# Kernel tuning notes

Hardware: AMD Instinct MI355X
Metric: run time of the kernel (lower is better)

The kernel has to match this reference:

```python
import jax, jax.numpy as jnp
import numpy as np

B, L, D, N = 4, 4096, 1024, 1024  # d_state must equal d_model for the original broadcasting to work


def _bayes_linear(x, wmu, wlv, bmu, blv, key):
    """Reparameterized Bayesian linear: w = mu + exp(0.5*log_var)*eps."""
    kw, kb = jax.random.split(key)
    w = wmu + jnp.exp(0.5 * wlv) * jax.random.normal(kw, wmu.shape, wmu.dtype)
    b = bmu + jnp.exp(0.5 * blv) * jax.random.normal(kb, bmu.shape, bmu.dtype)
    return x @ w.T + b


def setup_inputs() -> dict:
    key = jax.random.key(0)
    ks = jax.random.split(key, 17)
    inp = {"x": jax.random.normal(ks[0], (B, L, D), jnp.float32)}
    shapes = {"A": (N, D), "Bp": (N, D), "C": (D, N), "dt": (N, D)}
    i = 1
    for name, (o, ii) in shapes.items():
        # torch init: mu ~ N(0, 0.1), log_var ~ N(-9, 0.1)
        inp[f"{name}_wmu"] = 0.1 * jax.random.normal(ks[i], (o, ii), jnp.float32); i += 1
        inp[f"{name}_wlv"] = -9.0 + 0.1 * jax.random.normal(ks[i], (o, ii), jnp.float32); i += 1
        inp[f"{name}_bmu"] = 0.1 * jax.random.normal(ks[i], (o,), jnp.float32); i += 1
        inp[f"{name}_blv"] = -9.0 + 0.1 * jax.random.normal(ks[i], (o,), jnp.float32); i += 1
    return inp


def reference(x, A_wmu, A_wlv, A_bmu, A_blv,
              Bp_wmu, Bp_wlv, Bp_bmu, Bp_blv,
              C_wmu, C_wlv, C_bmu, C_blv,
              dt_wmu, dt_wlv, dt_bmu, dt_blv):
    key = jax.random.key(42)
    kA, kB, kC, kdt = jax.random.split(key, 4)
    A = -jnp.exp(_bayes_linear(x, A_wmu, A_wlv, A_bmu, A_blv, kA))   # [B,L,N]
    dt = jnp.exp(_bayes_linear(x, dt_wmu, dt_wlv, dt_bmu, dt_blv, kdt))
    Bm = _bayes_linear(x, Bp_wmu, Bp_wlv, Bp_bmu, Bp_blv, kB)        # [B,L,N]
    C = _bayes_linear(x, C_wmu, C_wlv, C_bmu, C_blv, kC)             # [B,L,D]

    E = jnp.exp(A * dt)   # per-step decay, [B,L,N]
    Bx = Bm * x           # input injection (requires N == D, as in original)

    def step(h, inp):
        e, bx, c = inp
        h = h * e + bx
        return h, c * h

    ET = jnp.swapaxes(E, 0, 1)    # time-major [L,B,N]
    BxT = jnp.swapaxes(Bx, 0, 1)
    CT = jnp.swapaxes(C, 0, 1)
    h0 = jnp.zeros((x.shape[0], N), x.dtype)
    _, yT = jax.lax.scan(step, h0, (ET, BxT, CT))
    # The torch code broadcasts h to [B,B,N] and sums over dim=1; h is identical
    # along that axis, so the sum equals multiplying by batch_size.
    return jnp.swapaxes(yT, 0, 1) * x.shape[0]
```

## Files before the change

kernel.cpp:

```cpp
#include <hip/hip_runtime.h>
#include <cstdint>

__host__ __device__ inline void tf2x32(uint32_t k0, uint32_t k1,
                                       uint32_t x0, uint32_t x1,
                                       uint32_t& o0, uint32_t& o1) {
  uint32_t ks2 = k0 ^ k1 ^ 0x1BD11BDAu;
  uint32_t v0 = x0 + k0, v1 = x1 + k1;
#define TFR(r) { v0 += v1; v1 = (v1 << r) | (v1 >> (32 - r)); v1 ^= v0; }
  TFR(13) TFR(15) TFR(26) TFR(6)
  v0 += k1;  v1 += ks2 + 1u;
  TFR(17) TFR(29) TFR(16) TFR(24)
  v0 += ks2; v1 += k0 + 2u;
  TFR(13) TFR(15) TFR(26) TFR(6)
  v0 += k0;  v1 += k1 + 3u;
  TFR(17) TFR(29) TFR(16) TFR(24)
  v0 += k1;  v1 += ks2 + 4u;
  TFR(13) TFR(15) TFR(26) TFR(6)
  v0 += ks2; v1 += k0 + 5u;
#undef TFR
  o0 = v0; o1 = v1;
}

__device__ inline float erfinv32(float x) {
  float w = -log1pf(-x * x);
  float p;
  if (w < 5.0f) {
    w -= 2.5f;
    p = 2.81022636e-08f;
    p = fmaf(p, w, 3.43273939e-07f);
    p = fmaf(p, w, -3.5233877e-06f);
    p = fmaf(p, w, -4.39150654e-06f);
    p = fmaf(p, w, 0.00021858087f);
    p = fmaf(p, w, -0.00125372503f);
    p = fmaf(p, w, -0.00417768164f);
    p = fmaf(p, w, 0.246640727f);
    p = fmaf(p, w, 1.50140941f);
  } else {
    w = sqrtf(w) - 3.0f;
    p = -0.000200214257f;
    p = fmaf(p, w, 0.000100950558f);
    p = fmaf(p, w, 0.00134934322f);
    p = fmaf(p, w, -0.00367342844f);
    p = fmaf(p, w, 0.00573950773f);
    p = fmaf(p, w, -0.0076224613f);
    p = fmaf(p, w, 0.00943887047f);
    p = fmaf(p, w, 1.00167406f);
    p = fmaf(p, w, 2.83297682f);
  }
  return p * x;
}

__device__ inline float rng_normal(uint32_t k0, uint32_t k1, uint32_t idx) {
  uint32_t o0, o1;
  tf2x32(k0, k1, 0u, idx, o0, o1);
  uint32_t bits = o0 ^ o1;
  float f = __uint_as_float((bits >> 9) | 0x3f800000u) - 1.0f;
  const float lo = -0.999999940395355224609375f;
  float u = fmaxf(lo, f * 2.0f + lo);
  return 1.41421356237f * erfinv32(u);
}

struct RngKeys {
  uint32_t wA0, wA1, bA0, bA1;
  uint32_t wB0, wB1, bB0, bB1;
  uint32_t wC0, wC1, bC0, bC1;
  uint32_t wD0, wD1, bD0, bD1;
};

typedef _Float16 f16x8 __attribute__((ext_vector_type(8)));
typedef _Float16 f16x4 __attribute__((ext_vector_type(4)));
typedef float f32x4 __attribute__((ext_vector_type(4)));

__global__ __launch_bounds__(256) void gen_weights(
    const float* __restrict__ Awmu, const float* __restrict__ Awlv,
    const float* __restrict__ Dwmu, const float* __restrict__ Dwlv,
    const float* __restrict__ Bwmu, const float* __restrict__ Bwlv,
    const float* __restrict__ Cwmu, const float* __restrict__ Cwlv,
    _Float16* __restrict__ Wh, RngKeys kk) {
  uint32_t idx = blockIdx.x * 256u + threadIdx.x;
  uint32_t sel = idx >> 20;
  uint32_t e = idx & 0xFFFFFu;
  float w;
  if (sel == 0u) {
    w = Awmu[e] + expf(0.5f * Awlv[e]) * rng_normal(kk.wA0, kk.wA1, e)
      + Dwmu[e] + expf(0.5f * Dwlv[e]) * rng_normal(kk.wD0, kk.wD1, e);
  } else if (sel == 1u) {
    w = Bwmu[e] + expf(0.5f * Bwlv[e]) * rng_normal(kk.wB0, kk.wB1, e);
  } else {
    w = Cwmu[e] + expf(0.5f * Cwlv[e]) * rng_normal(kk.wC0, kk.wC1, e);
  }
  Wh[idx] = (_Float16)w;
}

__global__ __launch_bounds__(256) void gen_bias(
    const float* __restrict__ Abmu, const float* __restrict__ Ablv,
    const float* __restrict__ Dbmu, const float* __restrict__ Dblv,
    const float* __restrict__ Bbmu, const float* __restrict__ Bblv,
    const float* __restrict__ Cbmu, const float* __restrict__ Cblv,
    float* __restrict__ bcat, RngKeys kk) {
  uint32_t o = blockIdx.x * 256u + threadIdx.x;
  uint32_t e = o & 1023u;
  float b;
  if (o < 1024u)
    b = Abmu[e] + expf(0.5f * Ablv[e]) * rng_normal(kk.bA0, kk.bA1, e)
      + Dbmu[e] + expf(0.5f * Dblv[e]) * rng_normal(kk.bD0, kk.bD1, e);
  else if (o < 2048u)
    b = Bbmu[e] + expf(0.5f * Bblv[e]) * rng_normal(kk.bB0, kk.bB1, e);
  else
    b = Cbmu[e] + expf(0.5f * Cblv[e]) * rng_normal(kk.bC0, kk.bC1, e);
  bcat[o] = b;
}

__global__ __launch_bounds__(256) void convert_x(const float* __restrict__ X,
                                                 _Float16* __restrict__ Xh) {
  size_t i4 = ((size_t)blockIdx.x * 256 + threadIdx.x) * 4;
  float4 v = *(const float4*)(X + i4);
  f16x4 h;
  h[0] = (_Float16)v.x; h[1] = (_Float16)v.y;
  h[2] = (_Float16)v.z; h[3] = (_Float16)v.w;
  *(f16x4*)(Xh + i4) = h;
}

__device__ inline void gl2lds16(const void* g, void* l) {
  __builtin_amdgcn_global_load_lds(
      (const __attribute__((address_space(1))) void*)g,
      (__attribute__((address_space(3))) void*)l, 16, 0, 0);
}

__global__ __launch_bounds__(256, 4) void gemm_fused(
    const _Float16* __restrict__ Xh, const _Float16* __restrict__ Wh,
    const float* __restrict__ X, const float* __restrict__ bcat,
    _Float16* __restrict__ Z, float* __restrict__ out) {
  __shared__ _Float16 sA[128 * 32];
  __shared__ _Float16 sB[128 * 32];

  const int tid = threadIdx.x;
  const int m0 = blockIdx.y * 128;
  const int n0 = blockIdx.x * 128;

  const int srow = tid >> 2;
  const int scg = (tid & 3) ^ ((srow >> 1) & 3);
  const _Float16* gA = Xh + (size_t)(m0 + srow) * 1024 + scg * 8;
  const _Float16* gB = Wh + (size_t)(n0 + srow) * 1024 + scg * 8;
  char* lA = (char*)sA + tid * 16;
  char* lB = (char*)sB + tid * 16;

  const int lane = tid & 63;
  const int wave = tid >> 6;
  const int wm = wave >> 1, wn = wave & 1;
  const int fr = lane & 15;
  const int q = lane >> 4;
  const int kc = q ^ ((fr >> 1) & 3);

  f32x4 acc[4][4] = {};

  for (int k0 = 0; k0 < 1024; k0 += 32) {
    __syncthreads();
    gl2lds16(gA + k0, lA);
    gl2lds16(gA + 64 * 1024 + k0, lA + 4096);
    gl2lds16(gB + k0, lB);
    gl2lds16(gB + 64 * 1024 + k0, lB + 4096);
    __syncthreads();

    f16x8 ah[4], bh[4];
#pragma unroll
    for (int t = 0; t < 4; ++t) {
      int ar = (wm * 64 + t * 16 + fr) * 32 + kc * 8;
      int br = (wn * 64 + t * 16 + fr) * 32 + kc * 8;
      ah[t] = *(const f16x8*)&sA[ar];
      bh[t] = *(const f16x8*)&sB[br];
    }
#pragma unroll
    for (int mt = 0; mt < 4; ++mt)
#pragma unroll
      for (int nt = 0; nt < 4; ++nt)
        acc[mt][nt] = __builtin_amdgcn_mfma_f32_16x16x32_f16(
            ah[mt], bh[nt], acc[mt][nt], 0, 0, 0);
  }

  const int seg = n0 >> 10;
  const int mrow = (lane >> 4) * 4;
#pragma unroll
  for (int nt = 0; nt < 4; ++nt) {
    int n = n0 + wn * 64 + nt * 16 + fr;
    float bv = bcat[n];
#pragma unroll
    for (int mt = 0; mt < 4; ++mt) {
      int mbase = m0 + wm * 64 + mt * 16 + mrow;
      f32x4 a = acc[mt][nt];
#pragma unroll
      for (int r = 0; r < 4; ++r) {
        int m = mbase + r;
        float v = a[r] + bv;
        if (seg == 0) {
          Z[(size_t)m * 2048 + n] = (_Float16)expf(-expf(v));
        } else if (seg == 1) {
          Z[(size_t)m * 2048 + n] =
              (_Float16)(v * X[(size_t)m * 1024 + (n - 1024)]);
        } else {
          out[(size_t)m * 1024 + (n - 2048)] = v;
        }
      }
    }
  }
}

#define LSEQ 4096
#define NC 64
#define LC 64
#define ZW 2048

__global__ __launch_bounds__(256) void scan_chunk(const _Float16* __restrict__ Z,
                                                  float* __restrict__ ac,
                                                  float* __restrict__ uc) {
  int n = blockIdx.x * 256 + threadIdx.x;
  int c = blockIdx.y;
  int b = blockIdx.z;
  const _Float16* base = Z + (size_t)(b * LSEQ + c * LC) * ZW;
  float a = 1.0f, u = 0.0f;
#pragma unroll 4
  for (int l = 0; l < LC; ++l) {
    float e  = (float)base[(size_t)l * ZW + n];
    float bx = (float)base[(size_t)l * ZW + 1024 + n];
    a *= e;
    u = fmaf(e, u, bx);
  }
  size_t o = ((size_t)b * NC + c) * 1024 + n;
  ac[o] = a;
  uc[o] = u;
}

__global__ __launch_bounds__(256) void scan_prefix(const float* __restrict__ ac,
                                                   const float* __restrict__ uc,
                                                   float* __restrict__ hin) {
  int idx = blockIdx.x * 256 + threadIdx.x;
  int b = idx >> 10, n = idx & 1023;
  float h = 0.0f;
  for (int c = 0; c < NC; ++c) {
    size_t o = ((size_t)b * NC + c) * 1024 + n;
    hin[o] = h;
    h = fmaf(ac[o], h, uc[o]);
  }
}

__global__ __launch_bounds__(256) void scan_final(const _Float16* __restrict__ Z,
                                                  const float* __restrict__ hin,
                                                  float* __restrict__ out) {
  int n = blockIdx.x * 256 + threadIdx.x;
  int c = blockIdx.y;
  int b = blockIdx.z;
  const _Float16* base = Z + (size_t)(b * LSEQ + c * LC) * ZW;
  float* obase = out + (size_t)(b * LSEQ + c * LC) * 1024;
  float h = hin[((size_t)b * NC + c) * 1024 + n];
#pragma unroll 4
  for (int l = 0; l < LC; ++l) {
    float e  = (float)base[(size_t)l * ZW + n];
    float bx = (float)base[(size_t)l * ZW + 1024 + n];
    float cc = obase[(size_t)l * 1024 + n];
    h = fmaf(e, h, bx);
    obase[(size_t)l * 1024 + n] = cc * h * 4.0f;
  }
}

extern "C" void kernel_launch(void* const* d_in, const int* in_sizes, int n_in,
                              void* d_out, int out_size, void* d_ws, size_t ws_size,
                              hipStream_t stream) {
  const float* x    = (const float*)d_in[0];
  const float* Awmu = (const float*)d_in[1];
  const float* Awlv = (const float*)d_in[2];
  const float* Abmu = (const float*)d_in[3];
  const float* Ablv = (const float*)d_in[4];
  const float* Bwmu = (const float*)d_in[5];
  const float* Bwlv = (const float*)d_in[6];
  const float* Bbmu = (const float*)d_in[7];
  const float* Bblv = (const float*)d_in[8];
  const float* Cwmu = (const float*)d_in[9];
  const float* Cwlv = (const float*)d_in[10];
  const float* Cbmu = (const float*)d_in[11];
  const float* Cblv = (const float*)d_in[12];
  const float* Dwmu = (const float*)d_in[13];
  const float* Dwlv = (const float*)d_in[14];
  const float* Dbmu = (const float*)d_in[15];
  const float* Dblv = (const float*)d_in[16];

  uint32_t k4[4][2];
  for (uint32_t i = 0; i < 4; ++i)
    tf2x32(0u, 42u, 0u, i, k4[i][0], k4[i][1]);
  RngKeys kk;
  tf2x32(k4[0][0], k4[0][1], 0u, 0u, kk.wA0, kk.wA1);
  tf2x32(k4[0][0], k4[0][1], 0u, 1u, kk.bA0, kk.bA1);
  tf2x32(k4[1][0], k4[1][1], 0u, 0u, kk.wB0, kk.wB1);
  tf2x32(k4[1][0], k4[1][1], 0u, 1u, kk.bB0, kk.bB1);
  tf2x32(k4[2][0], k4[2][1], 0u, 0u, kk.wC0, kk.wC1);
  tf2x32(k4[2][0], k4[2][1], 0u, 1u, kk.bC0, kk.bC1);
  tf2x32(k4[3][0], k4[3][1], 0u, 0u, kk.wD0, kk.wD1);
  tf2x32(k4[3][0], k4[3][1], 0u, 1u, kk.bD0, kk.bD1);

  char* ws = (char*)d_ws;
  const size_t OFF_WH   = 0;
  const size_t OFF_BCAT = 6291456;
  const size_t OFF_XH   = 8388608;
  const size_t OFF_Z    = 41943040;
  const size_t OFF_AC   = OFF_Z + (size_t)16384 * 2048 * 2;
  const size_t OFF_UC   = OFF_AC + (size_t)4 * NC * 1024 * 4;
  const size_t OFF_HIN  = OFF_UC + (size_t)4 * NC * 1024 * 4;
  const size_t NEEDED   = OFF_HIN + (size_t)4 * NC * 1024 * 4;
  if (ws_size < NEEDED) return;

  _Float16* Wh  = (_Float16*)(ws + OFF_WH);
  float*    bcat= (float*)(ws + OFF_BCAT);
  _Float16* Xh  = (_Float16*)(ws + OFF_XH);
  _Float16* Z   = (_Float16*)(ws + OFF_Z);
  float*    ac  = (float*)(ws + OFF_AC);
  float*    ucv = (float*)(ws + OFF_UC);
  float*    hin = (float*)(ws + OFF_HIN);
  float*    out = (float*)d_out;

  gen_weights<<<dim3(12288), dim3(256), 0, stream>>>(
      Awmu, Awlv, Dwmu, Dwlv, Bwmu, Bwlv, Cwmu, Cwlv, Wh, kk);
  gen_bias<<<dim3(12), dim3(256), 0, stream>>>(
      Abmu, Ablv, Dbmu, Dblv, Bbmu, Bblv, Cbmu, Cblv, bcat, kk);
  convert_x<<<dim3(16384), dim3(256), 0, stream>>>(x, Xh);
  gemm_fused<<<dim3(24, 128), dim3(256), 0, stream>>>(
      Xh, Wh, x, bcat, Z, out);
  scan_chunk<<<dim3(4, NC, 4), dim3(256), 0, stream>>>(Z, ac, ucv);
  scan_prefix<<<dim3(16), dim3(256), 0, stream>>>(ac, ucv, hin);
  scan_final<<<dim3(4, NC, 4), dim3(256), 0, stream>>>(Z, hin, out);
}
```

Measured before the change: 390.0 us.

## Restructure fused GEMM into 256x256 double-buffered tiles with ping-pong MFMA schedule

The projection GEMM moves from 128x128 tiles with BK=32 and one LDS buffer to 256x256 tiles with BK=64, double-buffered LDS and 512 threads per block. Each k-step is split into four MFMA quadrants, with global-to-LDS prefetch of the next tile interleaved, explicit barriers and setprio to overlap memory and matrix work. A block-index swizzle improves L2 reuse across tiles. The aim is higher arithmetic intensity and hidden load latency. The cost is 128KB of LDS per block, which caps occupancy at one block per CU, plus higher register pressure from the larger accumulator.

```diff
diff --git a/kernel.cpp b/kernel.cpp
--- a/kernel.cpp
+++ b/kernel.cpp
@@ -127,71 +127,152 @@
       (__attribute__((address_space(3))) void*)l, 16, 0, 0);
 }
 
-__global__ __launch_bounds__(256, 4) void gemm_fused(
+#define STAGE_T(S, GP, BUF, KT1)                              \
+  do {                                                        \
+    const _Float16* g_ = (GP) + (KT1) * 64;                   \
+    char* l_ = (char*)(&S[(BUF)][0]) + tid * 16;              \
+    gl2lds16(g_,              l_);                            \
+    gl2lds16(g_ +  64 * 1024, l_ + 8192);                     \
+    gl2lds16(g_ + 128 * 1024, l_ + 16384);                    \
+    gl2lds16(g_ + 192 * 1024, l_ + 24576);                    \
+  } while (0)
+
+#define READ_A(MH)                                                      \
+  do {                                                                  \
+    _Pragma("unroll") for (int k_ = 0; k_ < 4; ++k_) {                  \
+      const int ro_ = abase + ((MH) * 4 + k_) * 1024;                   \
+      ah[2 * k_]     = *(const f16x8*)&sA[cur][ro_ + apos];             \
+      ah[2 * k_ + 1] = *(const f16x8*)&sA[cur][ro_ + (apos ^ 32)];      \
+    }                                                                   \
+  } while (0)
+
+#define READ_B(NH)                                                      \
+  do {                                                                  \
+    _Pragma("unroll") for (int j_ = 0; j_ < 2; ++j_) {                  \
+      const int ro_ = bbase + ((NH) * 2 + j_) * 1024;                   \
+      bh[2 * j_]     = *(const f16x8*)&sB[cur][ro_ + apos];             \
+      bh[2 * j_ + 1] = *(const f16x8*)&sB[cur][ro_ + (apos ^ 32)];      \
+    }                                                                   \
+  } while (0)
+
+#define DO_MFMA(MH, NH)                                                      \
+  do {                                                                       \
+    _Pragma("unroll") for (int k_ = 0; k_ < 4; ++k_) {                       \
+      _Pragma("unroll") for (int j_ = 0; j_ < 2; ++j_) {                     \
+        f32x4 c_ = acc[(MH) * 4 + k_][(NH) * 2 + j_];                        \
+        c_ = __builtin_amdgcn_mfma_f32_16x16x32_f16(ah[2 * k_], bh[2 * j_],  \
+                                                    c_, 0, 0, 0);            \
+        c_ = __builtin_amdgcn_mfma_f32_16x16x32_f16(ah[2 * k_ + 1],          \
+                                                    bh[2 * j_ + 1], c_, 0,   \
+                                                    0, 0);                   \
+        acc[(MH) * 4 + k_][(NH) * 2 + j_] = c_;                              \
+      }                                                                      \
+    }                                                                        \
+  } while (0)
+
+#define SYNC_PRE()                                           \
+  do {                                                       \
+    __builtin_amdgcn_s_barrier();                            \
+    asm volatile("s_waitcnt lgkmcnt(0)" ::: "memory");       \
+    __builtin_amdgcn_sched_barrier(0);                       \
+    __builtin_amdgcn_s_setprio(1);                           \
+  } while (0)
+
+#define SYNC_POST()                                          \
+  do {                                                       \
+    __builtin_amdgcn_s_setprio(0);                           \
+    __builtin_amdgcn_s_barrier();                            \
+  } while (0)
+
+__global__ __launch_bounds__(512, 2) void gemm_fused(
     const _Float16* __restrict__ Xh, const _Float16* __restrict__ Wh,
     const float* __restrict__ X, const float* __restrict__ bcat,
     _Float16* __restrict__ Z, float* __restrict__ out) {
-  __shared__ _Float16 sA[128 * 32];
-  __shared__ _Float16 sB[128 * 32];
+  __shared__ _Float16 sA[2][256 * 64];
+  __shared__ _Float16 sB[2][256 * 64];
 
   const int tid = threadIdx.x;
-  const int m0 = blockIdx.y * 128;
-  const int n0 = blockIdx.x * 128;
-
-  const int srow = tid >> 2;
-  const int scg = (tid & 3) ^ ((srow >> 1) & 3);
-  const _Float16* gA = Xh + (size_t)(m0 + srow) * 1024 + scg * 8;
-  const _Float16* gB = Wh + (size_t)(n0 + srow) * 1024 + scg * 8;
-  char* lA = (char*)sA + tid * 16;
-  char* lB = (char*)sB + tid * 16;
+
+  const int swz = ((int)blockIdx.x & 7) * 96 + ((int)blockIdx.x >> 3);
+  const int mt = swz / 12;
+  const int nt = swz - mt * 12;
+  const int m0 = mt * 256;
+  const int n0 = nt * 256;
+
+  const int srow = tid >> 3;
+  const int sc = (tid & 7) ^ (srow & 7);
+  const _Float16* gA = Xh + (size_t)(m0 + srow) * 1024 + sc * 8;
+  const _Float16* gB = Wh + (size_t)(n0 + srow) * 1024 + sc * 8;
 
   const int lane = tid & 63;
   const int wave = tid >> 6;
-  const int wm = wave >> 1, wn = wave & 1;
+  const int wm = wave >> 2;
+  const int wn = wave & 3;
   const int fr = lane & 15;
   const int q = lane >> 4;
-  const int kc = q ^ ((fr >> 1) & 3);
-
-  f32x4 acc[4][4] = {};
-
-  for (int k0 = 0; k0 < 1024; k0 += 32) {
-    __syncthreads();
-    gl2lds16(gA + k0, lA);
-    gl2lds16(gA + 64 * 1024 + k0, lA + 4096);
-    gl2lds16(gB + k0, lB);
-    gl2lds16(gB + 64 * 1024 + k0, lB + 4096);
-    __syncthreads();
-
-    f16x8 ah[4], bh[4];
-#pragma unroll
-    for (int t = 0; t < 4; ++t) {
-      int ar = (wm * 64 + t * 16 + fr) * 32 + kc * 8;
-      int br = (wn * 64 + t * 16 + fr) * 32 + kc * 8;
-      ah[t] = *(const f16x8*)&sA[ar];
-      bh[t] = *(const f16x8*)&sB[br];
-    }
-#pragma unroll
-    for (int mt = 0; mt < 4; ++mt)
-#pragma unroll
-      for (int nt = 0; nt < 4; ++nt)
-        acc[mt][nt] = __builtin_amdgcn_mfma_f32_16x16x32_f16(
-            ah[mt], bh[nt], acc[mt][nt], 0, 0, 0);
+  const int f7 = fr & 7;
+
+  const int abase = wm * 8192 + fr * 64;
+  const int bbase = wn * 4096 + fr * 64;
+  const int apos = (q ^ f7) * 8;
+
+  f32x4 acc[8][4] = {};
+  f16x8 ah[8], bh[4];
+
+  STAGE_T(sA, gA, 0, 0);
+  STAGE_T(sB, gB, 0, 0);
+  asm volatile("s_waitcnt vmcnt(0)" ::: "memory");
+  __builtin_amdgcn_s_barrier();
+
+  for (int kt = 0; kt < 16; ++kt) {
+    const int cur = kt & 1;
+    const int nxt = cur ^ 1;
+    const bool pf = (kt < 15);
+
+    if (pf) STAGE_T(sA, gA, nxt, kt + 1);
+    READ_A(0);
+    READ_B(0);
+    SYNC_PRE();
+    DO_MFMA(0, 0);
+    SYNC_POST();
+
+    if (pf) STAGE_T(sB, gB, nxt, kt + 1);
+    READ_B(1);
+    SYNC_PRE();
+    DO_MFMA(0, 1);
+    SYNC_POST();
+
+    READ_A(1);
+    SYNC_PRE();
+    DO_MFMA(1, 1);
+    SYNC_POST();
+
+    READ_B(0);
+    __builtin_amdgcn_s_barrier();
+    asm volatile("s_waitcnt lgkmcnt(0)" ::: "memory");
+    __builtin_amdgcn_sched_barrier(0);
+    __builtin_amdgcn_s_setprio(1);
+    DO_MFMA(1, 0);
+    __builtin_amdgcn_s_setprio(0);
+    asm volatile("s_waitcnt vmcnt(0)" ::: "memory");
+    __builtin_amdgcn_s_barrier();
   }
 
   const int seg = n0 >> 10;
   const int mrow = (lane >> 4) * 4;
+  const int mb0 = m0 + wm * 128;
 #pragma unroll
-  for (int nt = 0; nt < 4; ++nt) {
-    int n = n0 + wn * 64 + nt * 16 + fr;
-    float bv = bcat[n];
+  for (int nf = 0; nf < 4; ++nf) {
+    const int n = n0 + wn * 64 + nf * 16 + fr;
+    const float bv = bcat[n];
 #pragma unroll
-    for (int mt = 0; mt < 4; ++mt) {
-      int mbase = m0 + wm * 64 + mt * 16 + mrow;
-      f32x4 a = acc[mt][nt];
+    for (int mf = 0; mf < 8; ++mf) {
+      const int mbase = mb0 + mf * 16 + mrow;
+      f32x4 a = acc[mf][nf];
 #pragma unroll
       for (int r = 0; r < 4; ++r) {
-        int m = mbase + r;
-        float v = a[r] + bv;
+        const int m = mbase + r;
+        const float v = a[r] + bv;
         if (seg == 0) {
           Z[(size_t)m * 2048 + n] = (_Float16)expf(-expf(v));
         } else if (seg == 1) {
@@ -321,7 +402,7 @@
   gen_bias<<<dim3(12), dim3(256), 0, stream>>>(
       Abmu, Ablv, Dbmu, Dblv, Bbmu, Bblv, Cbmu, Cblv, bcat, kk);
   convert_x<<<dim3(16384), dim3(256), 0, stream>>>(x, Xh);
-  gemm_fused<<<dim3(24, 128), dim3(256), 0, stream>>>(
+  gemm_fused<<<dim3(768), dim3(512), 0, stream>>>(
       Xh, Wh, x, bcat, Z, out);
   scan_chunk<<<dim3(4, NC, 4), dim3(256), 0, stream>>>(Z, ac, ucv);
   scan_prefix<<<dim3(16), dim3(256), 0, stream>>>(ac, ucv, hin);
```

Result: slower. 445.4 us (+14.2%).

## Restructure fused GEMM into 256x256 double-buffered tiles with XCD-aware block swizzle

Applied to the files above, without the earlier changes.

The projection GEMM moves from 128x128 tiles with 256 threads and a single LDS buffer to 256x256 tiles with 512 threads. The K loop is now double-buffered with async global-to-LDS loads, split into two 32-wide halves per 64-wide K step, and synchronised with explicit vmcnt waits and barriers. A block-index swizzle groups tiles per XCD, and s_setprio is raised around the MFMA bursts. The aim is more data reuse per loaded byte and overlap of loads with MFMA work. The trade-offs are higher register and LDS pressure, and the loss of the previous XOR LDS swizzle, which may bring back bank conflicts.

```diff
diff --git a/kernel.cpp b/kernel.cpp
--- a/kernel.cpp
+++ b/kernel.cpp
@@ -127,71 +127,106 @@
       (__attribute__((address_space(3))) void*)l, 16, 0, 0);
 }
 
-__global__ __launch_bounds__(256, 4) void gemm_fused(
+#define STAGE_U(BUF, KT, KC)                                   \
+  do {                                                         \
+    const _Float16* ga_ = gA + (KT) * 64 + (KC) * 32;          \
+    const _Float16* gb_ = gB + (KT) * 64 + (KC) * 32;          \
+    char* la_ = (char*)(&sA[(BUF)][(KC)][0]) + tid * 16;       \
+    char* lb_ = (char*)(&sB[(BUF)][(KC)][0]) + tid * 16;       \
+    gl2lds16(ga_, la_);                                        \
+    gl2lds16(ga_ + 128 * 1024, la_ + 8192);                    \
+    gl2lds16(gb_, lb_);                                        \
+    gl2lds16(gb_ + 128 * 1024, lb_ + 8192);                    \
+  } while (0)
+
+#define HALF_TILE(CUR, KC)                                                    \
+  do {                                                                        \
+    _Pragma("unroll") for (int mf_ = 0; mf_ < 8; ++mf_)                       \
+      ah[mf_] =                                                               \
+          *(const f16x8*)&sA[(CUR)][(KC)][(abase + mf_ * 16) * 32 + qo];      \
+    _Pragma("unroll") for (int nf_ = 0; nf_ < 4; ++nf_)                       \
+      bh[nf_] =                                                               \
+          *(const f16x8*)&sB[(CUR)][(KC)][(bbase + nf_ * 16) * 32 + qo];      \
+    asm volatile("s_waitcnt lgkmcnt(0)" ::: "memory");                        \
+    __builtin_amdgcn_sched_barrier(0);                                        \
+    __builtin_amdgcn_s_setprio(1);                                            \
+    _Pragma("unroll") for (int mf_ = 0; mf_ < 8; ++mf_)                       \
+      _Pragma("unroll") for (int nf_ = 0; nf_ < 4; ++nf_)                     \
+        acc[mf_][nf_] = __builtin_amdgcn_mfma_f32_16x16x32_f16(               \
+            ah[mf_], bh[nf_], acc[mf_][nf_], 0, 0, 0);                        \
+    __builtin_amdgcn_s_setprio(0);                                            \
+  } while (0)
+
+__global__ __launch_bounds__(512, 2) void gemm_fused(
     const _Float16* __restrict__ Xh, const _Float16* __restrict__ Wh,
     const float* __restrict__ X, const float* __restrict__ bcat,
     _Float16* __restrict__ Z, float* __restrict__ out) {
-  __shared__ _Float16 sA[128 * 32];
-  __shared__ _Float16 sB[128 * 32];
+  __shared__ _Float16 sA[2][2][256 * 32];
+  __shared__ _Float16 sB[2][2][256 * 32];
 
   const int tid = threadIdx.x;
-  const int m0 = blockIdx.y * 128;
-  const int n0 = blockIdx.x * 128;
-
-  const int srow = tid >> 2;
-  const int scg = (tid & 3) ^ ((srow >> 1) & 3);
-  const _Float16* gA = Xh + (size_t)(m0 + srow) * 1024 + scg * 8;
-  const _Float16* gB = Wh + (size_t)(n0 + srow) * 1024 + scg * 8;
-  char* lA = (char*)sA + tid * 16;
-  char* lB = (char*)sB + tid * 16;
+
+  const int swz = ((int)blockIdx.x & 7) * 96 + ((int)blockIdx.x >> 3);
+  const int mt = swz / 12;
+  const int nt = swz - mt * 12;
+  const int m0 = mt * 256;
+  const int n0 = nt * 256;
+
+  const _Float16* gA = Xh + (size_t)(m0 + (tid >> 2)) * 1024 + (tid & 3) * 8;
+  const _Float16* gB = Wh + (size_t)(n0 + (tid >> 2)) * 1024 + (tid & 3) * 8;
 
   const int lane = tid & 63;
   const int wave = tid >> 6;
-  const int wm = wave >> 1, wn = wave & 1;
+  const int wm = wave >> 2;
+  const int wn = wave & 3;
   const int fr = lane & 15;
-  const int q = lane >> 4;
-  const int kc = q ^ ((fr >> 1) & 3);
-
-  f32x4 acc[4][4] = {};
-
-  for (int k0 = 0; k0 < 1024; k0 += 32) {
-    __syncthreads();
-    gl2lds16(gA + k0, lA);
-    gl2lds16(gA + 64 * 1024 + k0, lA + 4096);
-    gl2lds16(gB + k0, lB);
-    gl2lds16(gB + 64 * 1024 + k0, lB + 4096);
-    __syncthreads();
-
-    f16x8 ah[4], bh[4];
-#pragma unroll
-    for (int t = 0; t < 4; ++t) {
-      int ar = (wm * 64 + t * 16 + fr) * 32 + kc * 8;
-      int br = (wn * 64 + t * 16 + fr) * 32 + kc * 8;
-      ah[t] = *(const f16x8*)&sA[ar];
-      bh[t] = *(const f16x8*)&sB[br];
-    }
-#pragma unroll
-    for (int mt = 0; mt < 4; ++mt)
-#pragma unroll
-      for (int nt = 0; nt < 4; ++nt)
-        acc[mt][nt] = __builtin_amdgcn_mfma_f32_16x16x32_f16(
-            ah[mt], bh[nt], acc[mt][nt], 0, 0, 0);
-  }
+  const int qo = (lane >> 4) * 8;
+
+  const int abase = wm * 128 + fr;
+  const int bbase = wn * 64 + fr;
+
+  f32x4 acc[8][4] = {};
+  f16x8 ah[8], bh[4];
+
+  STAGE_U(0, 0, 0);
+  STAGE_U(0, 0, 1);
+
+  for (int kt = 0; kt < 15; ++kt) {
+    const int cur = kt & 1;
+    const int nxt = cur ^ 1;
+    STAGE_U(nxt, kt + 1, 0);
+    asm volatile("s_waitcnt vmcnt(8)" ::: "memory");
+    __builtin_amdgcn_s_barrier();
+    HALF_TILE(cur, 0);
+    STAGE_U(nxt, kt + 1, 1);
+    asm volatile("s_waitcnt vmcnt(8)" ::: "memory");
+    __builtin_amdgcn_s_barrier();
+    HALF_TILE(cur, 1);
+    __builtin_amdgcn_s_barrier();
+  }
+  asm volatile("s_waitcnt vmcnt(4)" ::: "memory");
+  __builtin_amdgcn_s_barrier();
+  HALF_TILE(1, 0);
+  asm volatile("s_waitcnt vmcnt(0)" ::: "memory");
+  __builtin_amdgcn_s_barrier();
+  HALF_TILE(1, 1);
+  __builtin_amdgcn_sched_barrier(0);
 
   const int seg = n0 >> 10;
   const int mrow = (lane >> 4) * 4;
+  const int mb0 = m0 + wm * 128;
 #pragma unroll
-  for (int nt = 0; nt < 4; ++nt) {
-    int n = n0 + wn * 64 + nt * 16 + fr;
-    float bv = bcat[n];
+  for (int nf = 0; nf < 4; ++nf) {
+    const int n = n0 + wn * 64 + nf * 16 + fr;
+    const float bv = bcat[n];
 #pragma unroll
-    for (int mt = 0; mt < 4; ++mt) {
-      int mbase = m0 + wm * 64 + mt * 16 + mrow;
-      f32x4 a = acc[mt][nt];
+    for (int mf = 0; mf < 8; ++mf) {
+      const int mbase = mb0 + mf * 16 + mrow;
+      f32x4 a = acc[mf][nf];
 #pragma unroll
       for (int r = 0; r < 4; ++r) {
-        int m = mbase + r;
-        float v = a[r] + bv;
+        const int m = mbase + r;
+        const float v = a[r] + bv;
         if (seg == 0) {
           Z[(size_t)m * 2048 + n] = (_Float16)expf(-expf(v));
         } else if (seg == 1) {
@@ -321,7 +356,7 @@
   gen_bias<<<dim3(12), dim3(256), 0, stream>>>(
       Abmu, Ablv, Dbmu, Dblv, Bbmu, Bblv, Cbmu, Cblv, bcat, kk);
   convert_x<<<dim3(16384), dim3(256), 0, stream>>>(x, Xh);
-  gemm_fused<<<dim3(24, 128), dim3(256), 0, stream>>>(
+  gemm_fused<<<dim3(768), dim3(512), 0, stream>>>(
       Xh, Wh, x, bcat, Z, out);
   scan_chunk<<<dim3(4, NC, 4), dim3(256), 0, stream>>>(Z, ac, ucv);
   scan_prefix<<<dim3(16), dim3(256), 0, stream>>>(ac, ucv, hin);
```

Result: slower. 433.1 us (+11.0%).

## Swizzle GEMM block order and vectorize scan kernels to four channels per thread

Applied to the files above, without the earlier changes.

Remaps the GEMM block index with an XCD-aware swizzle so that consecutive blocks on the same chiplet share M tiles, aiming for better L2 reuse. The scan_chunk and scan_final kernels now handle four channels per thread using f16x4 and float4 loads and stores. Their grids shrink to 256 blocks to match. A small unroll pragma is added to scan_prefix. Vectorizing the scans cuts the number of memory instructions, but each thread now carries four serial recurrences and there are fewer threads in flight, which may lower latency hiding.

```diff
diff --git a/kernel.cpp b/kernel.cpp
--- a/kernel.cpp
+++ b/kernel.cpp
@@ -135,8 +135,13 @@
   __shared__ _Float16 sB[128 * 32];
 
   const int tid = threadIdx.x;
-  const int m0 = blockIdx.y * 128;
-  const int n0 = blockIdx.x * 128;
+
+  const int bid = (int)blockIdx.y * 24 + (int)blockIdx.x;
+  const int swz = (bid & 7) * 384 + (bid >> 3);
+  const int mt = swz / 24;
+  const int nt = swz - mt * 24;
+  const int m0 = mt * 128;
+  const int n0 = nt * 128;
 
   const int srow = tid >> 2;
   const int scg = (tid & 3) ^ ((srow >> 1) & 3);
@@ -171,23 +176,23 @@
       bh[t] = *(const f16x8*)&sB[br];
     }
 #pragma unroll
-    for (int mt = 0; mt < 4; ++mt)
-#pragma unroll
-      for (int nt = 0; nt < 4; ++nt)
-        acc[mt][nt] = __builtin_amdgcn_mfma_f32_16x16x32_f16(
-            ah[mt], bh[nt], acc[mt][nt], 0, 0, 0);
+    for (int mtt = 0; mtt < 4; ++mtt)
+#pragma unroll
+      for (int ntt = 0; ntt < 4; ++ntt)
+        acc[mtt][ntt] = __builtin_amdgcn_mfma_f32_16x16x32_f16(
+            ah[mtt], bh[ntt], acc[mtt][ntt], 0, 0, 0);
   }
 
   const int seg = n0 >> 10;
   const int mrow = (lane >> 4) * 4;
 #pragma unroll
-  for (int nt = 0; nt < 4; ++nt) {
-    int n = n0 + wn * 64 + nt * 16 + fr;
+  for (int ntt = 0; ntt < 4; ++ntt) {
+    int n = n0 + wn * 64 + ntt * 16 + fr;
     float bv = bcat[n];
 #pragma unroll
-    for (int mt = 0; mt < 4; ++mt) {
-      int mbase = m0 + wm * 64 + mt * 16 + mrow;
-      f32x4 a = acc[mt][nt];
+    for (int mtt = 0; mtt < 4; ++mtt) {
+      int mbase = m0 + wm * 64 + mtt * 16 + mrow;
+      f32x4 a = acc[mtt][ntt];
 #pragma unroll
       for (int r = 0; r < 4; ++r) {
         int m = mbase + r;
@@ -213,21 +218,26 @@
 __global__ __launch_bounds__(256) void scan_chunk(const _Float16* __restrict__ Z,
                                                   float* __restrict__ ac,
                                                   float* __restrict__ uc) {
-  int n = blockIdx.x * 256 + threadIdx.x;
+  int n4 = threadIdx.x * 4;
   int c = blockIdx.y;
   int b = blockIdx.z;
   const _Float16* base = Z + (size_t)(b * LSEQ + c * LC) * ZW;
-  float a = 1.0f, u = 0.0f;
+  float a[4] = {1.0f, 1.0f, 1.0f, 1.0f};
+  float u[4] = {0.0f, 0.0f, 0.0f, 0.0f};
 #pragma unroll 4
   for (int l = 0; l < LC; ++l) {
-    float e  = (float)base[(size_t)l * ZW + n];
-    float bx = (float)base[(size_t)l * ZW + 1024 + n];
-    a *= e;
-    u = fmaf(e, u, bx);
-  }
-  size_t o = ((size_t)b * NC + c) * 1024 + n;
-  ac[o] = a;
-  uc[o] = u;
+    f16x4 ev = *(const f16x4*)&base[(size_t)l * ZW + n4];
+    f16x4 bx = *(const f16x4*)&base[(size_t)l * ZW + 1024 + n4];
+#pragma unroll
+    for (int i = 0; i < 4; ++i) {
+      float e = (float)ev[i];
+      a[i] *= e;
+      u[i] = fmaf(e, u[i], (float)bx[i]);
+    }
+  }
+  size_t o = ((size_t)b * NC + c) * 1024 + n4;
+  *(float4*)&ac[o] = make_float4(a[0], a[1], a[2], a[3]);
+  *(float4*)&uc[o] = make_float4(u[0], u[1], u[2], u[3]);
 }
 
 __global__ __launch_bounds__(256) void scan_prefix(const float* __restrict__ ac,
@@ -236,6 +246,7 @@
   int idx = blockIdx.x * 256 + threadIdx.x;
   int b = idx >> 10, n = idx & 1023;
   float h = 0.0f;
+#pragma unroll 8
   for (int c = 0; c < NC; ++c) {
     size_t o = ((size_t)b * NC + c) * 1024 + n;
     hin[o] = h;
@@ -246,19 +257,25 @@
 __global__ __launch_bounds__(256) void scan_final(const _Float16* __restrict__ Z,
                                                   const float* __restrict__ hin,
                                                   float* __restrict__ out) {
-  int n = blockIdx.x * 256 + threadIdx.x;
+  int n4 = threadIdx.x * 4;
   int c = blockIdx.y;
   int b = blockIdx.z;
   const _Float16* base = Z + (size_t)(b * LSEQ + c * LC) * ZW;
   float* obase = out + (size_t)(b * LSEQ + c * LC) * 1024;
-  float h = hin[((size_t)b * NC + c) * 1024 + n];
+  size_t ho = ((size_t)b * NC + c) * 1024 + n4;
+  float4 hv = *(const float4*)&hin[ho];
+  float h[4] = {hv.x, hv.y, hv.z, hv.w};
 #pragma unroll 4
   for (int l = 0; l < LC; ++l) {
-    float e  = (float)base[(size_t)l * ZW + n];
-    float bx = (float)base[(size_t)l * ZW + 1024 + n];
-    float cc = obase[(size_t)l * 1024 + n];
-    h = fmaf(e, h, bx);
-    obase[(size_t)l * 1024 + n] = cc * h * 4.0f;
+    f16x4 ev = *(const f16x4*)&base[(size_t)l * ZW + n4];
+    f16x4 bx = *(const f16x4*)&base[(size_t)l * ZW + 1024 + n4];
+    float4 cc = *(const float4*)&obase[(size_t)l * 1024 + n4];
+#pragma unroll
+    for (int i = 0; i < 4; ++i)
+      h[i] = fmaf((float)ev[i], h[i], (float)bx[i]);
+    *(float4*)&obase[(size_t)l * 1024 + n4] =
+        make_float4(cc.x * h[0] * 4.0f, cc.y * h[1] * 4.0f,
+                    cc.z * h[2] * 4.0f, cc.w * h[3] * 4.0f);
   }
 }
 
@@ -323,7 +340,7 @@
   convert_x<<<dim3(16384), dim3(256), 0, stream>>>(x, Xh);
   gemm_fused<<<dim3(24, 128), dim3(256), 0, stream>>>(
       Xh, Wh, x, bcat, Z, out);
-  scan_chunk<<<dim3(4, NC, 4), dim3(256), 0, stream>>>(Z, ac, ucv);
+  scan_chunk<<<dim3(1, NC, 4), dim3(256), 0, stream>>>(Z, ac, ucv);
   scan_prefix<<<dim3(16), dim3(256), 0, stream>>>(ac, ucv, hin);
-  scan_final<<<dim3(4, NC, 4), dim3(256), 0, stream>>>(Z, hin, out);
-}
+  scan_final<<<dim3(1, NC, 4), dim3(256), 0, stream>>>(Z, hin, out);
+}
```

Result: slower. 403.3 us (+3.4%).
